# Kernel optimization log

Hardware: AMD Instinct MI355X
Metric: run time of the kernel (lower is better)

The kernel has to match this reference:

```python
import jax, jax.numpy as jnp
import numpy as np

B = 4096
HASH_BITS = 128
TEACHER_DIM = 768
TEMPERATURE = 0.2
CONTRASTIVE_W = 1.0
DISTILL_W = 0.5
QUANT_W = 0.01


def _l2_normalize(x, eps=1e-12):
    # matches torch F.normalize(dim=-1)
    n = jnp.sqrt(jnp.sum(x * x, axis=-1, keepdims=True))
    return x / jnp.maximum(n, eps)


def setup_inputs() -> dict:
    key = jax.random.key(0)
    k1, k2, k3, k4 = jax.random.split(key, 4)
    logits = jax.random.normal(k1, (B, HASH_BITS), dtype=jnp.float32)
    # binary {-1,+1} codes as in the module contract
    hash_codes = jnp.sign(jax.random.normal(k2, (B, HASH_BITS), dtype=jnp.float32))
    hash_codes = jnp.where(hash_codes == 0, 1.0, hash_codes)
    teacher_embed = jax.random.normal(k3, (B, TEACHER_DIM), dtype=jnp.float32)
    # sparse random positives plus self-positives (guarantees each row nonempty)
    rand_pos = jax.random.uniform(k4, (B, B)) < 0.002
    eye = jnp.eye(B, dtype=bool)
    positive_mask = rand_pos | eye
    return {
        "logits": logits,
        "hash_codes": hash_codes,
        "teacher_embed": teacher_embed,
        "positive_mask": positive_mask,
    }


def reference(logits, hash_codes, teacher_embed, positive_mask):
    teacher = _l2_normalize(teacher_embed)

    # ---- contrastive (vectorized form of the per-row python loop) ----
    ln = _l2_normalize(logits)
    sim = (ln @ ln.T) / TEMPERATURE  # [B, B]
    eye = jnp.eye(sim.shape[0], dtype=bool)
    sim_masked = jnp.where(eye, -jnp.inf, sim)
    # per-row stable logsumexp over self-masked similarities
    log_denom = jax.nn.logsumexp(sim_masked, axis=1)  # [B]
    pm = positive_mask.astype(sim.dtype)
    cnt = pm.sum(axis=1)  # [B]
    pos_mean = (sim * pm).sum(axis=1) / jnp.maximum(cnt, 1.0)
    has_pos = cnt > 0
    per_row = jnp.where(has_pos, -pos_mean + log_denom, 0.0)
    num_pos = jnp.maximum(has_pos.sum(), 1)
    loss_cont = per_row.sum() / num_pos.astype(sim.dtype)

    # ---- distillation: hash similarity vs teacher similarity MSE ----
    hash_sim = (hash_codes @ hash_codes.T) / hash_codes.shape[-1]
    teacher_sim = teacher @ teacher.T
    loss_distill = jnp.mean((hash_sim - teacher_sim) ** 2)

    # ---- quantization: push |logits| toward 1 ----
    loss_quant = jnp.mean(jnp.abs(jnp.abs(logits) - 1.0))

    total = (
        CONTRASTIVE_W * loss_cont
        + DISTILL_W * loss_distill
        + QUANT_W * loss_quant
    )
    return total
```

## Files before the change

kernel.cpp:

```cpp
#include <hip/hip_runtime.h>


typedef __bf16 bf16x8 __attribute__((ext_vector_type(8)));
typedef float f32x4 __attribute__((ext_vector_type(4)));

__device__ __forceinline__ unsigned short f2bf(float f) {
  union { float f; unsigned int u; } v; v.f = f;
  unsigned int u = v.u;
  return (unsigned short)((u + 0x7FFFu + ((u >> 16) & 1u)) >> 16);
}

__device__ __forceinline__ void atomAddF(float* p, float v) {
  unsafeAtomicAdd(p, v);
}
__device__ __forceinline__ float atomReadF(float* p) {
  return unsafeAtomicAdd(p, 0.f);
}

__global__ __launch_bounds__(256) void prep(const float* __restrict__ logits,
                                            const float* __restrict__ hash,
                                            const float* __restrict__ teacher,
                                            unsigned short* __restrict__ P,
                                            unsigned char* __restrict__ QT,
                                            float* __restrict__ qpart,
                                            float* __restrict__ rowexp,
                                            float* __restrict__ possum,
                                            float* __restrict__ cntw,
                                            float* __restrict__ accs,
                                            float* __restrict__ Cbuf) {
  __shared__ float rnt[8];
  __shared__ unsigned char QL[8 * 897];
  const int t = threadIdx.x, wave = t >> 6, lane = t & 63;
  const int r0 = (int)blockIdx.x * 8;

  for (int i = t; i < 224; i += 256)
    *(f32x4*)&Cbuf[((size_t)blockIdx.x * 224 + i) * 4] = (f32x4){0.f, 0.f, 0.f, 0.f};
  if (blockIdx.x == 0) {
    if (t < 4) accs[t] = 0.f;
    if (t == 4) *(int*)&accs[4] = 0;
  }

#pragma unroll
  for (int rr = 0; rr < 2; ++rr) {
    const int rl = wave * 2 + rr, r = r0 + rl;
    float ss = 0.f;
#pragma unroll
    for (int i = 0; i < 3; ++i) {
      const float4 v = *(const float4*)&teacher[(size_t)r * 768 + i * 256 + lane * 4];
      ss += v.x * v.x + v.y * v.y + v.z * v.z + v.w * v.w;
    }
    const float2 lv = *(const float2*)&logits[(size_t)r * 128 + lane * 2];
    float ssl = lv.x * lv.x + lv.y * lv.y;
    float qv = fabsf(fabsf(lv.x) - 1.f) + fabsf(fabsf(lv.y) - 1.f);
#pragma unroll
    for (int off = 1; off < 64; off <<= 1) {
      ss += __shfl_xor(ss, off, 64);
      ssl += __shfl_xor(ssl, off, 64);
      qv += __shfl_xor(qv, off, 64);
    }
    const float rnl = 1.f / fmaxf(sqrtf(ssl), 1e-12f);
    const unsigned int pk = (unsigned int)f2bf(lv.x * rnl) |
                            ((unsigned int)f2bf(lv.y * rnl) << 16);
    *(unsigned int*)&P[(size_t)r * 128 + lane * 2] = pk;
    if (lane == 0) {
      rnt[rl] = 11.313708498984761f / fmaxf(sqrtf(ss), 1e-12f);
      qpart[r] = qv;
    }
  }
  if (t < 8) { rowexp[r0 + t] = 0.f; possum[r0 + t] = 0.f; cntw[r0 + t] = 0.f; }
  __syncthreads();

#pragma unroll
  for (int it = 0; it < 2; ++it) {
    const int task = it * 256 + t;
    if (task < 448) {
      const int r = task / 56, cb = task % 56;
      const int r_g = r0 + r;
      unsigned char* dst = &QL[r * 897 + cb * 16];
      if (cb < 8) {
        const float4 v0 = *(const float4*)&hash[(size_t)r_g * 128 + cb * 16];
        const float4 v1 = *(const float4*)&hash[(size_t)r_g * 128 + cb * 16 + 4];
        const float4 v2 = *(const float4*)&hash[(size_t)r_g * 128 + cb * 16 + 8];
        const float4 v3 = *(const float4*)&hash[(size_t)r_g * 128 + cb * 16 + 12];
        const float vv[16] = {v0.x, v0.y, v0.z, v0.w, v1.x, v1.y, v1.z, v1.w,
                              v2.x, v2.y, v2.z, v2.w, v3.x, v3.y, v3.z, v3.w};
#pragma unroll
        for (int k = 0; k < 16; ++k) dst[k] = vv[k] >= 0.f ? 0x38 : 0xB8;
      } else {
        const float sc = rnt[r];
        const int c0 = cb * 16 - 128;
        const float4 v0 = *(const float4*)&teacher[(size_t)r_g * 768 + c0];
        const float4 v1 = *(const float4*)&teacher[(size_t)r_g * 768 + c0 + 4];
        const float4 v2 = *(const float4*)&teacher[(size_t)r_g * 768 + c0 + 8];
        const float4 v3 = *(const float4*)&teacher[(size_t)r_g * 768 + c0 + 12];
        const float vv[16] = {v0.x, v0.y, v0.z, v0.w, v1.x, v1.y, v1.z, v1.w,
                              v2.x, v2.y, v2.z, v2.w, v3.x, v3.y, v3.z, v3.w};
#pragma unroll
        for (int k = 0; k < 16; ++k) {
          const int p8 = __builtin_amdgcn_cvt_pk_fp8_f32(vv[k] * sc, vv[k] * sc,
                                                         0, false);
          dst[k] = (unsigned char)(p8 & 0xFF);
        }
      }
    }
  }
  __syncthreads();

#pragma unroll
  for (int i = 0; i < 4; ++i) {
    const int c = t + 256 * i;
    if (c < 896) {
      unsigned char buf[8];
#pragma unroll
      for (int j = 0; j < 8; ++j) buf[j] = QL[j * 897 + c];
      *(uint2*)&QT[(size_t)c * 4096 + r0] = *(uint2*)buf;
    }
  }
}

#define STAGE_GEN(GA, GB, PITCH, BASE)                                         \
  {                                                                            \
    _Pragma("unroll") for (int it = 0; it < 4; ++it) {                         \
      const int task = it * 256 + t;                                           \
      const int row = task >> 3;                                               \
      const int c16 = (task & 7) ^ (row & 7);                                  \
      const unsigned char* gpA = (GA) + (size_t)row * (PITCH) + c16 * 16;      \
      __builtin_amdgcn_global_load_lds(                                        \
          (const __attribute__((address_space(1))) void*)gpA,                  \
          (__attribute__((address_space(3))) void*)                            \
              &SB[(BASE) + it * 4096 + wave * 1024],                           \
          16, 0, 0);                                                           \
      if (offdiag) {                                                           \
        const unsigned char* gpB = (GB) + (size_t)row * (PITCH) + c16 * 16;    \
        __builtin_amdgcn_global_load_lds(                                      \
            (const __attribute__((address_space(1))) void*)gpB,                \
            (__attribute__((address_space(3))) void*)                         \
                &SB[(BASE) + 16384 + it * 4096 + wave * 1024],                 \
            16, 0, 0);                                                         \
      }                                                                        \
    }                                                                          \
  }

#define MFMA_B(BASE)                                                           \
  {                                                                            \
    _Pragma("unroll") for (int ks = 0; ks < 2; ++ks) {                         \
      const int ph = ((ks * 4 + qd) ^ (l15 & 7)) * 16;                         \
      bf16x8 af[4], bfr[4];                                                    \
      _Pragma("unroll") for (int rt = 0; rt < 4; ++rt)                         \
          af[rt] = *(const bf16x8*)&SB[(BASE) +                                \
                                       (wy * 64 + rt * 16 + l15) * 128 + ph];  \
      _Pragma("unroll") for (int ct = 0; ct < 4; ++ct)                         \
          bfr[ct] = *(const bf16x8*)&SB[(BASE) + boffB +                       \
                                        (wx * 64 + ct * 16 + l15) * 128 + ph]; \
      _Pragma("unroll") for (int rt = 0; rt < 4; ++rt)                         \
          _Pragma("unroll") for (int ct = 0; ct < 4; ++ct) acc[rt][ct] =       \
          __builtin_amdgcn_mfma_f32_16x16x32_bf16(af[rt], bfr[ct],             \
                                                  acc[rt][ct], 0, 0, 0);       \
    }                                                                          \
  }

#define MFMA_Q(BASE)                                                           \
  {                                                                            \
    _Pragma("unroll") for (int ks = 0; ks < 4; ++ks) {                         \
      const int g0 = ks * 4 + qd;                                              \
      const int ph = ((g0 >> 1) ^ (l15 & 7)) * 16 + (g0 & 1) * 8;              \
      long af[4], bfr[4];                                                      \
      _Pragma("unroll") for (int rt = 0; rt < 4; ++rt)                         \
          af[rt] = *(const long*)&SB[(BASE) +                                  \
                                     (wy * 64 + rt * 16 + l15) * 128 + ph];    \
      _Pragma("unroll") for (int ct = 0; ct < 4; ++ct)                         \
          bfr[ct] = *(const long*)&SB[(BASE) + boffB +                         \
                                      (wx * 64 + ct * 16 + l15) * 128 + ph];   \
      _Pragma("unroll") for (int rt = 0; rt < 4; ++rt)                         \
          _Pragma("unroll") for (int ct = 0; ct < 4; ++ct) acc[rt][ct] =       \
          __builtin_amdgcn_mfma_f32_16x16x32_fp8_fp8(af[rt], bfr[ct],          \
                                                     acc[rt][ct], 0, 0, 0);    \
    }                                                                          \
  }

__global__ __launch_bounds__(256, 2) void mega(const unsigned short* __restrict__ P,
                                               const unsigned char* __restrict__ QT,
                                               const void* __restrict__ mask,
                                               float* __restrict__ rowexp,
                                               float* __restrict__ possum,
                                               float* __restrict__ cntw,
                                               float* __restrict__ Cbuf) {
  __shared__ __align__(16) unsigned char SB[65536];
  __shared__ float redrow[128][2];
  __shared__ float redcol[128][2];

  const int t = threadIdx.x;
  const int wave = t >> 6, lane = t & 63;
  const int qd = lane >> 4, l15 = lane & 15;
  const int wy = wave >> 1, wx = wave & 1;
  const int b = (int)blockIdx.x;

  f32x4 acc[4][4];
#pragma unroll
  for (int rt = 0; rt < 4; ++rt)
#pragma unroll
    for (int ct = 0; ct < 4; ++ct) acc[rt][ct] = {0.f, 0.f, 0.f, 0.f};

  if (b < 112) {
    const int tile = b >> 2, ksl = b & 3;
    int I = 0, rem = tile;
    while (rem >= 7 - I) { rem -= 7 - I; ++I; }
    const int J = I + rem;
    const bool offdiag = (I != J);
    const int boffB = offdiag ? 16384 : 0;
    const unsigned char* QA = QT + (size_t)I * 128 * 4096 + ksl * 1024;
    const unsigned char* QB = QT + (size_t)J * 128 * 4096 + ksl * 1024;

    STAGE_GEN(QA, QB, 4096, 0);
    __syncthreads();
    for (int kc = 0; kc < 8; ++kc) {
      const int cb = (kc & 1) * 32768;
      if (kc < 7) STAGE_GEN(QA + (kc + 1) * 128, QB + (kc + 1) * 128, 4096,
                            cb ^ 32768);
      MFMA_Q(cb);
      __syncthreads();
    }
    float* Ct = Cbuf + (size_t)tile * 16384;
#pragma unroll
    for (int rt = 0; rt < 4; ++rt)
#pragma unroll
      for (int ct = 0; ct < 4; ++ct)
#pragma unroll
        for (int i = 0; i < 4; ++i)
          atomAddF(&Ct[(rt * 4 + ct) * 1024 + i * 256 + t], acc[rt][ct][i]);
  } else {
    const int bb = b - 112;
    const int l = (bb & 7) * 66 + (bb >> 3);
    int I = 0, rem = l;
    while (rem >= 32 - I) { rem -= 32 - I; ++I; }
    const int bi = I, bj = I + rem;
    const int ti = bi * 128, tj = bj * 128;
    const bool offdiag = (bi != bj);
    const int boffB = offdiag ? 16384 : 0;
    const bool is_byte = ((const unsigned char*)mask)[4097] != 0;

    const unsigned char* Pa = (const unsigned char*)(P + (size_t)ti * 128);
    const unsigned char* Pb = (const unsigned char*)(P + (size_t)tj * 128);

    STAGE_GEN(Pa, Pb, 256, 0);
    __syncthreads();
    STAGE_GEN(Pa + 128, Pb + 128, 256, 32768);
    MFMA_B(0);
    __syncthreads();
    if (is_byte) {
      const unsigned char* m8 = (const unsigned char*)mask;
      const unsigned char* m8d = m8 + (size_t)ti * 4096 + tj;
      const unsigned char* m8t = m8 + (size_t)tj * 4096 + ti;
#pragma unroll
      for (int it = 0; it < 4; ++it) {
        const int task = it * 256 + t;
        const int row = task >> 3, seg = task & 7;
        __builtin_amdgcn_global_load_lds(
            (const __attribute__((address_space(1))) void*)
                (m8d + (size_t)row * 4096 + seg * 16),
            (__attribute__((address_space(3))) void*)&SB[it * 4096 + wave * 1024],
            16, 0, 0);
        if (offdiag)
          __builtin_amdgcn_global_load_lds(
              (const __attribute__((address_space(1))) void*)
                  (m8t + (size_t)row * 4096 + seg * 16),
              (__attribute__((address_space(3))) void*)
                  &SB[16384 + it * 4096 + wave * 1024],
              16, 0, 0);
      }
    }
    MFMA_B(32768);
    __syncthreads();
    if (!is_byte) {
      const unsigned int* m32 = (const unsigned int*)mask;
#pragma unroll
      for (int it = 0; it < 16; ++it) {
        const int task = it * 256 + t;
        const int row = task >> 5, seg = task & 31;
        const uint4 v = *(const uint4*)&m32[(size_t)(ti + row) * 4096 + tj + seg * 4];
        uchar4 pk;
        pk.x = v.x ? 1 : 0; pk.y = v.y ? 1 : 0;
        pk.z = v.z ? 1 : 0; pk.w = v.w ? 1 : 0;
        *(uchar4*)&SB[row * 128 + seg * 4] = pk;
        if (offdiag) {
          const uint4 w = *(const uint4*)&m32[(size_t)(tj + row) * 4096 + ti + seg * 4];
          uchar4 pw;
          pw.x = w.x ? 1 : 0; pw.y = w.y ? 1 : 0;
          pw.z = w.z ? 1 : 0; pw.w = w.w ? 1 : 0;
          *(uchar4*)&SB[16384 + row * 128 + seg * 4] = pw;
        }
      }
      __syncthreads();
    }

    float ce[4] = {0.f, 0.f, 0.f, 0.f};
#pragma unroll
    for (int rt = 0; rt < 4; ++rt) {
#pragma unroll
      for (int r = 0; r < 4; ++r) {
        const int mrow = wy * 64 + rt * 16 + qd * 4 + r;
        const int m = ti + mrow;
        float se = 0.f;
#pragma unroll
        for (int ct = 0; ct < 4; ++ct) {
          const int ncol = wx * 64 + ct * 16 + l15;
          const int n = tj + ncol;
          const float sim = acc[rt][ct][r] * 5.0f;
          const float e = __expf(sim);
          if (m != n) se += e;
          if (offdiag) ce[ct] += e;
          if (SB[mrow * 128 + ncol]) {
            atomAddF(&possum[m], sim);
            atomAddF(&cntw[m], 1.0f);
          }
          if (offdiag && SB[16384 + ncol * 128 + mrow]) {
            atomAddF(&possum[n], sim);
            atomAddF(&cntw[n], 1.0f);
          }
        }
#pragma unroll
        for (int off = 1; off < 16; off <<= 1) se += __shfl_xor(se, off, 64);
        if (l15 == 0) redrow[mrow][wx] = se;
      }
    }
    if (offdiag) {
#pragma unroll
      for (int ct = 0; ct < 4; ++ct) {
        float c = ce[ct];
        c += __shfl_xor(c, 16, 64);
        c += __shfl_xor(c, 32, 64);
        if (qd == 0) redcol[wx * 64 + ct * 16 + l15][wy] = c;
      }
    }
    __syncthreads();
    if (t < 128) {
      atomAddF(&rowexp[ti + t], redrow[t][0] + redrow[t][1]);
      if (offdiag) atomAddF(&rowexp[tj + t], redcol[t][0] + redcol[t][1]);
    }
  }
}

__global__ __launch_bounds__(256) void reduce(const float* __restrict__ rowexp,
                                              const float* __restrict__ possum,
                                              const float* __restrict__ cnt,
                                              const float* __restrict__ qpart,
                                              const float* __restrict__ Cbuf,
                                              float* __restrict__ accs,
                                              float* __restrict__ out) {
  const int t = threadIdx.x;
  const int wave = t >> 6, lane = t & 63;
  const int g = (int)blockIdx.x * 256 + t;

  float c = 0.f, q = 0.f, d = 0.f;
  if (g < 4096) {
    c = logf(rowexp[g]) - possum[g] / fmaxf(cnt[g], 1.0f);
    q = qpart[g];
  }
#pragma unroll
  for (int k = 0; k < 7; ++k) {
    const int e4 = g + k * 16384;
    const int tile = e4 >> 12;
    int I = 0, rem = tile;
    while (rem >= 7 - I) { rem -= 7 - I; ++I; }
    const int J = I + rem;
    const float w = (I == J ? 1.f : 2.f) * (((I == 0) == (J == 0)) ? 1.f : -1.f);
    const f32x4 v = *(const f32x4*)&Cbuf[(size_t)e4 * 4];
    d += w * (v[0] * v[0] + v[1] * v[1] + v[2] * v[2] + v[3] * v[3]);
  }
#pragma unroll
  for (int off = 1; off < 64; off <<= 1) {
    c += __shfl_xor(c, off, 64);
    q += __shfl_xor(q, off, 64);
    d += __shfl_xor(d, off, 64);
  }
  __shared__ float sc[4], sq[4], sd[4];
  if (lane == 0) { sc[wave] = c; sq[wave] = q; sd[wave] = d; }
  __syncthreads();
  if (t == 0) {
    atomAddF(&accs[0], sc[0] + sc[1] + sc[2] + sc[3]);
    atomAddF(&accs[1], sq[0] + sq[1] + sq[2] + sq[3]);
    atomAddF(&accs[2], sd[0] + sd[1] + sd[2] + sd[3]);
    __threadfence();
    const int old = atomicAdd((int*)&accs[4], 1);
    if (old == 63) {
      __threadfence();
      const float C = atomReadF(&accs[0]);
      const float Q = atomReadF(&accs[1]);
      const float D = atomReadF(&accs[2]);
      out[0] = C * (1.0f / 4096.0f) + 0.5f * (D * 3.6379788e-12f) +
               0.01f * (Q * (1.0f / 524288.0f));
    }
  }
}

extern "C" void kernel_launch(void* const* d_in, const int* in_sizes, int n_in,
                              void* d_out, int out_size, void* d_ws, size_t ws_size,
                              hipStream_t stream) {
  const float* logits = (const float*)d_in[0];
  const float* hash = (const float*)d_in[1];
  const float* teacher = (const float*)d_in[2];
  const void* mask = d_in[3];
  float* out = (float*)d_out;

  char* ws = (char*)d_ws;
  float* rowexp = (float*)(ws + 0);
  float* possum = (float*)(ws + 16384);
  float* cntw = (float*)(ws + 32768);
  float* qpart = (float*)(ws + 49152);
  float* accs = (float*)(ws + 65536);
  unsigned short* P = (unsigned short*)(ws + 98304);
  unsigned char* QT = (unsigned char*)(ws + 98304 + 1048576);
  float* Cbuf = (float*)(ws + 98304 + 1048576 + 3670016);

  prep<<<512, 256, 0, stream>>>(logits, hash, teacher, P, QT, qpart, rowexp,
                                possum, cntw, accs, Cbuf);
  mega<<<640, 256, 0, stream>>>(P, QT, mask, rowexp, possum, cntw, Cbuf);
  reduce<<<64, 256, 0, stream>>>(rowexp, possum, cntw, qpart, Cbuf, accs, out);
}
```

Before: 176.2 us.

## Bit-pack positive mask in prep kernel and read bits in contrastive tiles

The prep kernel now reads the full positive mask once and packs it into a 1-bit-per-entry matrix, handling both byte and int32 mask formats. The contrastive tiles in the main kernel then read 64-bit words of this packed mask straight from global memory into registers. This replaces the per-tile LDS staging of the byte/int mask and removes a barrier. The cost is a dense pass over the 16M-entry mask in prep plus extra workspace, traded for far less mask traffic and LDS work in the main kernel.

```diff
diff --git a/kernel.cpp b/kernel.cpp
--- a/kernel.cpp
+++ b/kernel.cpp
@@ -20,8 +20,10 @@
 __global__ __launch_bounds__(256) void prep(const float* __restrict__ logits,
                                             const float* __restrict__ hash,
                                             const float* __restrict__ teacher,
+                                            const void* __restrict__ mask,
                                             unsigned short* __restrict__ P,
                                             unsigned char* __restrict__ QT,
+                                            unsigned char* __restrict__ PMb,
                                             float* __restrict__ qpart,
                                             float* __restrict__ rowexp,
                                             float* __restrict__ possum,
@@ -38,6 +40,35 @@
   if (blockIdx.x == 0) {
     if (t < 4) accs[t] = 0.f;
     if (t == 4) *(int*)&accs[4] = 0;
+  }
+
+  const bool is_byte = ((const unsigned char*)mask)[4097] != 0;
+  if (is_byte) {
+    const unsigned char* m8 = (const unsigned char*)mask;
+#pragma unroll
+    for (int it = 0; it < 8; ++it) {
+      const uint4 v = *(const uint4*)&m8[(size_t)(r0 + it) * 4096 + t * 16];
+      const unsigned char* bp = (const unsigned char*)&v;
+      unsigned int b = 0;
+#pragma unroll
+      for (int k = 0; k < 16; ++k) b |= (bp[k] ? 1u : 0u) << k;
+      *(unsigned short*)&PMb[(size_t)(r0 + it) * 512 + t * 2] = (unsigned short)b;
+    }
+  } else {
+    const unsigned int* m32 = (const unsigned int*)mask;
+#pragma unroll
+    for (int it = 0; it < 8; ++it) {
+      unsigned int b = 0;
+#pragma unroll
+      for (int q = 0; q < 4; ++q) {
+        const uint4 v = *(const uint4*)&m32[(size_t)(r0 + it) * 4096 + t * 16 + q * 4];
+        b |= (v.x ? 1u : 0u) << (q * 4);
+        b |= (v.y ? 1u : 0u) << (q * 4 + 1);
+        b |= (v.z ? 1u : 0u) << (q * 4 + 2);
+        b |= (v.w ? 1u : 0u) << (q * 4 + 3);
+      }
+      *(unsigned short*)&PMb[(size_t)(r0 + it) * 512 + t * 2] = (unsigned short)b;
+    }
   }
 
 #pragma unroll
@@ -180,7 +211,7 @@
 
 __global__ __launch_bounds__(256, 2) void mega(const unsigned short* __restrict__ P,
                                                const unsigned char* __restrict__ QT,
-                                               const void* __restrict__ mask,
+                                               const unsigned char* __restrict__ PMb,
                                                float* __restrict__ rowexp,
                                                float* __restrict__ possum,
                                                float* __restrict__ cntw,
@@ -237,7 +268,6 @@
     const int ti = bi * 128, tj = bj * 128;
     const bool offdiag = (bi != bj);
     const int boffB = offdiag ? 16384 : 0;
-    const bool is_byte = ((const unsigned char*)mask)[4097] != 0;
 
     const unsigned char* Pa = (const unsigned char*)(P + (size_t)ti * 128);
     const unsigned char* Pb = (const unsigned char*)(P + (size_t)tj * 128);
@@ -247,50 +277,15 @@
     STAGE_GEN(Pa + 128, Pb + 128, 256, 32768);
     MFMA_B(0);
     __syncthreads();
-    if (is_byte) {
-      const unsigned char* m8 = (const unsigned char*)mask;
-      const unsigned char* m8d = m8 + (size_t)ti * 4096 + tj;
-      const unsigned char* m8t = m8 + (size_t)tj * 4096 + ti;
-#pragma unroll
-      for (int it = 0; it < 4; ++it) {
-        const int task = it * 256 + t;
-        const int row = task >> 3, seg = task & 7;
-        __builtin_amdgcn_global_load_lds(
-            (const __attribute__((address_space(1))) void*)
-                (m8d + (size_t)row * 4096 + seg * 16),
-            (__attribute__((address_space(3))) void*)&SB[it * 4096 + wave * 1024],
-            16, 0, 0);
-        if (offdiag)
-          __builtin_amdgcn_global_load_lds(
-              (const __attribute__((address_space(1))) void*)
-                  (m8t + (size_t)row * 4096 + seg * 16),
-              (__attribute__((address_space(3))) void*)
-                  &SB[16384 + it * 4096 + wave * 1024],
-              16, 0, 0);
+    MFMA_B(32768);
+
+    unsigned long long Mt[4] = {0ull, 0ull, 0ull, 0ull};
+    if (offdiag) {
+#pragma unroll
+      for (int ct = 0; ct < 4; ++ct) {
+        const int n = tj + wx * 64 + ct * 16 + l15;
+        Mt[ct] = *(const unsigned long long*)&PMb[(size_t)n * 512 + (ti >> 3) + wy * 8];
       }
-    }
-    MFMA_B(32768);
-    __syncthreads();
-    if (!is_byte) {
-      const unsigned int* m32 = (const unsigned int*)mask;
-#pragma unroll
-      for (int it = 0; it < 16; ++it) {
-        const int task = it * 256 + t;
-        const int row = task >> 5, seg = task & 31;
-        const uint4 v = *(const uint4*)&m32[(size_t)(ti + row) * 4096 + tj + seg * 4];
-        uchar4 pk;
-        pk.x = v.x ? 1 : 0; pk.y = v.y ? 1 : 0;
-        pk.z = v.z ? 1 : 0; pk.w = v.w ? 1 : 0;
-        *(uchar4*)&SB[row * 128 + seg * 4] = pk;
-        if (offdiag) {
-          const uint4 w = *(const uint4*)&m32[(size_t)(tj + row) * 4096 + ti + seg * 4];
-          uchar4 pw;
-          pw.x = w.x ? 1 : 0; pw.y = w.y ? 1 : 0;
-          pw.z = w.z ? 1 : 0; pw.w = w.w ? 1 : 0;
-          *(uchar4*)&SB[16384 + row * 128 + seg * 4] = pw;
-        }
-      }
-      __syncthreads();
     }
 
     float ce[4] = {0.f, 0.f, 0.f, 0.f};
@@ -300,6 +295,8 @@
       for (int r = 0; r < 4; ++r) {
         const int mrow = wy * 64 + rt * 16 + qd * 4 + r;
         const int m = ti + mrow;
+        const unsigned long long Md =
+            *(const unsigned long long*)&PMb[(size_t)m * 512 + (tj >> 3) + wx * 8];
         float se = 0.f;
 #pragma unroll
         for (int ct = 0; ct < 4; ++ct) {
@@ -309,11 +306,11 @@
           const float e = __expf(sim);
           if (m != n) se += e;
           if (offdiag) ce[ct] += e;
-          if (SB[mrow * 128 + ncol]) {
+          if ((Md >> (ct * 16 + l15)) & 1ull) {
             atomAddF(&possum[m], sim);
             atomAddF(&cntw[m], 1.0f);
           }
-          if (offdiag && SB[16384 + ncol * 128 + mrow]) {
+          if (offdiag && ((Mt[ct] >> (rt * 16 + qd * 4 + r)) & 1ull)) {
             atomAddF(&possum[n], sim);
             atomAddF(&cntw[n], 1.0f);
           }
@@ -410,10 +407,11 @@
   float* accs = (float*)(ws + 65536);
   unsigned short* P = (unsigned short*)(ws + 98304);
   unsigned char* QT = (unsigned char*)(ws + 98304 + 1048576);
-  float* Cbuf = (float*)(ws + 98304 + 1048576 + 3670016);
-
-  prep<<<512, 256, 0, stream>>>(logits, hash, teacher, P, QT, qpart, rowexp,
-                                possum, cntw, accs, Cbuf);
-  mega<<<640, 256, 0, stream>>>(P, QT, mask, rowexp, possum, cntw, Cbuf);
+  float* Cbuf = (float*)(ws + 4816896);
+  unsigned char* PMb = (unsigned char*)(ws + 6651904);
+
+  prep<<<512, 256, 0, stream>>>(logits, hash, teacher, mask, P, QT, PMb, qpart,
+                                rowexp, possum, cntw, accs, Cbuf);
+  mega<<<640, 256, 0, stream>>>(P, QT, PMb, rowexp, possum, cntw, Cbuf);
   reduce<<<64, 256, 0, stream>>>(rowexp, possum, cntw, qpart, Cbuf, accs, out);
 }
```

Measured after the change: 155.9 us. 1.13x faster.
